# Kernel tuning notes

Measured on AMD Instinct MI355X. Metric: run time of the kernel, lower is better.

## Reference

```python
import jax, jax.numpy as jnp
import numpy as np

B, C, H, W = 32, 512, 24, 8
C8 = C // 8  # PAM query/key channels


def setup_inputs() -> dict:
    key = jax.random.key(0)
    k0, k1, k2, k3, k4 = jax.random.split(key, 5)
    x = jax.random.normal(k0, (B, C, H, W), dtype=jnp.float32)
    Wq = jax.random.normal(k1, (C8, C), dtype=jnp.float32) * 0.02
    bq = jnp.zeros((C8,), dtype=jnp.float32)
    Wk = jax.random.normal(k2, (C8, C), dtype=jnp.float32) * 0.02
    bk = jnp.zeros((C8,), dtype=jnp.float32)
    return {"x": x, "Wq": Wq, "bq": bq, "Wk": Wk, "bk": bk}


def reference(x, Wq, bq, Wk, bk):
    b, c, h, w = x.shape
    hw = h * w
    xf = x.reshape(b, c, hw)  # [B, C, hw]

    # QAConv: einsum('gchw,pcyx->gpyxhw') with kernel == x, then view(B,-1,hw,hw).
    # With m=(h,w) of features and n=(y,x) of kernel this is 'gcm,pcn->gpnm'.
    score = jnp.einsum('gcm,pcn->gpnm', xf, xf)  # [B, B, hw, hw]
    kernel_max = score.max(axis=3)               # max over feature positions -> [B, B, hw]

    # PAM: 1x1 conv projections then bmm(q^T, k).
    q = jnp.einsum('qc,bcm->bqm', Wq, xf) + bq[None, :, None]  # [B, C8, hw]
    k = jnp.einsum('qc,bcm->bqm', Wk, xf) + bk[None, :, None]  # [B, C8, hw]
    energy = jnp.einsum('bqm,bqn->bmn', q, k)                  # [B, hw, hw]
    pos_max = energy.max(axis=2)[None]                         # [1, B, hw]

    return jnp.concatenate([kernel_max, pos_max], axis=0)  # [B+1, B, hw]
```

## Files before the change

### kernel.cpp

```cpp
#include <hip/hip_runtime.h>

typedef __bf16 bf16x8 __attribute__((ext_vector_type(8)));
typedef float f32x4 __attribute__((ext_vector_type(4)));
typedef unsigned short u16x8 __attribute__((ext_vector_type(8)));
typedef unsigned short u16x4 __attribute__((ext_vector_type(4)));

#define B_ 32
#define CC 512
#define HW 192
#define C8_ 64
#define NTRI 528
#define PAIR_B 24576
#define SMEM_BYTES 73728

__device__ inline unsigned short f2bf(float f) {
    unsigned u = __float_as_uint(f);
    unsigned r = (u + 0x7FFFu + ((u >> 16) & 1u)) >> 16;
    return (unsigned short)r;
}

__device__ inline void gload16(const void* g, void* l) {
    __builtin_amdgcn_global_load_lds(
        (const __attribute__((address_space(1))) unsigned*)g,
        (__attribute__((address_space(3))) unsigned*)l,
        16, 0, 0);
}

__global__ void k_transpose(const float* __restrict__ x,
                            unsigned short* __restrict__ xt) {
    __shared__ unsigned short tile[64 * 64];
    int b = blockIdx.x / 3, mt = blockIdx.x % 3;
    int m0 = mt * 64, c0 = blockIdx.y * 64;
    int t = threadIdx.x;
    const float* xb = x + (size_t)b * CC * HW + (size_t)c0 * HW + m0;

    int mq = t & 15, cl0 = t >> 4;
    int sw = (mq & 7) << 3;
    #pragma unroll
    for (int rd = 0; rd < 4; ++rd) {
        int cl = rd * 16 + cl0;
        f32x4 v = *(const f32x4*)(xb + cl * HW + mq * 4);
        #pragma unroll
        for (int e = 0; e < 4; ++e)
            tile[(mq * 4 + e) * 64 + (cl ^ sw)] = f2bf(v[e]);
    }
    __syncthreads();
    unsigned short* xo = xt + ((size_t)b * HW + m0) * CC + c0;
    int kc = t & 7, mr0 = t >> 3;
    #pragma unroll
    for (int rd = 0; rd < 2; ++rd) {
        int mr = rd * 32 + mr0;
        u16x8 v = *(const u16x8*)&tile[mr * 64 + ((kc << 3) ^ (((mr >> 2) & 7) << 3))];
        *(u16x8*)(xo + (size_t)mr * CC + kc * 8) = v;
    }
}

__global__ void wcvt(const float* __restrict__ Wq, const float* __restrict__ Wk,
                     unsigned short* __restrict__ wqb, unsigned short* __restrict__ wkb) {
    const float* src = (blockIdx.x < 32) ? Wq : Wk;
    unsigned short* dst = (blockIdx.x < 32) ? wqb : wkb;
    int base = (blockIdx.x & 31) * 1024 + threadIdx.x * 4;
    f32x4 a = *(const f32x4*)(src + base);
    u16x4 o;
    #pragma unroll
    for (int e = 0; e < 4; ++e) o[e] = f2bf(a[e]);
    *(u16x4*)(dst + base) = o;
}

__global__ __launch_bounds__(256) void pam_qk(
        const unsigned short* __restrict__ xt,
        const unsigned short* __restrict__ wqb, const unsigned short* __restrict__ wkb,
        const float* __restrict__ bq, const float* __restrict__ bk,
        unsigned short* __restrict__ qo, unsigned short* __restrict__ ko) {
    int b = blockIdx.x, m0 = blockIdx.y * 48;
    int tid = threadIdx.x, w = tid >> 6, lane = tid & 63;
    int l15 = lane & 15, lq = lane >> 4;
    int qc = w * 16 + l15;

    f32x4 accq[3], acck[3];
    #pragma unroll
    for (int i = 0; i < 3; ++i) {
        accq[i] = (f32x4){0.f, 0.f, 0.f, 0.f};
        acck[i] = (f32x4){0.f, 0.f, 0.f, 0.f};
    }

    const unsigned short* xb = xt + ((size_t)b * HW + m0) * CC;
    const unsigned short* wqp = wqb + (size_t)qc * CC;
    const unsigned short* wkp = wkb + (size_t)qc * CC;

    for (int kt = 0; kt < 16; ++kt) {
        int ko8 = kt * 32 + lq * 8;
        bf16x8 wqf = *(const bf16x8*)(wqp + ko8);
        bf16x8 wkf = *(const bf16x8*)(wkp + ko8);
        bf16x8 af[3];
        #pragma unroll
        for (int i = 0; i < 3; ++i)
            af[i] = *(const bf16x8*)(xb + (i * 16 + l15) * CC + ko8);
        #pragma unroll
        for (int i = 0; i < 3; ++i) {
            accq[i] = __builtin_amdgcn_mfma_f32_16x16x32_bf16(af[i], wqf, accq[i], 0, 0, 0);
            acck[i] = __builtin_amdgcn_mfma_f32_16x16x32_bf16(af[i], wkf, acck[i], 0, 0, 0);
        }
    }

    float bqv = bq[qc], bkv = bk[qc];
    #pragma unroll
    for (int i = 0; i < 3; ++i) {
        #pragma unroll
        for (int r = 0; r < 4; ++r) {
            int m = m0 + i * 16 + lq * 4 + r;
            qo[((size_t)b * HW + m) * C8_ + qc] = f2bf(accq[i][r] + bqv);
            ko[((size_t)b * HW + m) * C8_ + qc] = f2bf(acck[i][r] + bkv);
        }
    }
}

__global__ __launch_bounds__(256) void pam_energy(
        const unsigned short* __restrict__ qo,
        const unsigned short* __restrict__ ko,
        float* __restrict__ out) {
    int b = blockIdx.x, m0 = blockIdx.y * 48;
    int tid = threadIdx.x, w = tid >> 6, lane = tid & 63;
    int l15 = lane & 15, lq = lane >> 4;
    int n0 = w * 48;

    f32x4 acc[3][3];
    #pragma unroll
    for (int i = 0; i < 3; ++i)
        #pragma unroll
        for (int j = 0; j < 3; ++j)
            acc[i][j] = (f32x4){0.f, 0.f, 0.f, 0.f};

    const unsigned short* qb = qo + ((size_t)b * HW + m0) * C8_;
    const unsigned short* kb = ko + ((size_t)b * HW + n0) * C8_;

    #pragma unroll
    for (int kt = 0; kt < 2; ++kt) {
        int ko8 = kt * 32 + lq * 8;
        bf16x8 af[3], bfr[3];
        #pragma unroll
        for (int i = 0; i < 3; ++i)
            af[i] = *(const bf16x8*)(qb + (i * 16 + l15) * C8_ + ko8);
        #pragma unroll
        for (int j = 0; j < 3; ++j)
            bfr[j] = *(const bf16x8*)(kb + (j * 16 + l15) * C8_ + ko8);
        #pragma unroll
        for (int i = 0; i < 3; ++i)
            #pragma unroll
            for (int j = 0; j < 3; ++j)
                acc[i][j] = __builtin_amdgcn_mfma_f32_16x16x32_bf16(af[i], bfr[j], acc[i][j], 0, 0, 0);
    }

    __shared__ float red[4][48];
    #pragma unroll
    for (int i = 0; i < 3; ++i) {
        float rm[4];
        #pragma unroll
        for (int r = 0; r < 4; ++r) rm[r] = -1e30f;
        #pragma unroll
        for (int j = 0; j < 3; ++j)
            #pragma unroll
            for (int r = 0; r < 4; ++r)
                rm[r] = fmaxf(rm[r], acc[i][j][r]);
        #pragma unroll
        for (int msk = 1; msk <= 8; msk <<= 1)
            #pragma unroll
            for (int r = 0; r < 4; ++r)
                rm[r] = fmaxf(rm[r], __shfl_xor(rm[r], msk));
        if (l15 == 0) {
            #pragma unroll
            for (int r = 0; r < 4; ++r)
                red[w][i * 16 + lq * 4 + r] = rm[r];
        }
    }
    __syncthreads();
    if (tid < 48) {
        float v = fmaxf(fmaxf(red[0][tid], red[1][tid]),
                        fmaxf(red[2][tid], red[3][tid]));
        out[((size_t)B_ * B_ + b) * HW + m0 + tid] = v;
    }
}

__global__ __launch_bounds__(512, 4) void gram(const unsigned short* __restrict__ xt,
                                               float* __restrict__ out) {
    extern __shared__ char smem[];

    int tid = threadIdx.x;
    int bid = (blockIdx.x & 7) * 66 + (blockIdx.x >> 3);
    int idx = bid, g = 0;
    while (idx >= B_ - g) { idx -= B_ - g; ++g; }
    int p = g + idx;

    const unsigned short* xg = xt + (size_t)g * HW * CC;
    const unsigned short* xp = xt + (size_t)p * HW * CC;

    int w = tid >> 6, lane = tid & 63;
    int wr = w >> 2, wc = w & 3;
    int l15 = lane & 15, lq = lane >> 4;

    int rowbase = (w & 3) * 48;
    const unsigned short* gsrc = (w < 4 ? xg : xp)
        + (size_t)(rowbase + (lane >> 2)) * CC
        + (((lane & 3) ^ ((lane >> 3) & 3)) << 3);
    unsigned ldsoff = (unsigned)(w < 4 ? 0 : 12288) + (unsigned)rowbase * 64;

    unsigned ssw = (unsigned)((lq ^ ((l15 >> 1) & 3)) << 4);
    unsigned aoff[6], boff[3];
    #pragma unroll
    for (int i = 0; i < 6; ++i)
        aoff[i] = (unsigned)(wr * 96 + i * 16 + l15) * 64 + ssw;
    #pragma unroll
    for (int j = 0; j < 3; ++j)
        boff[j] = 12288u + (unsigned)(wc * 48 + j * 16 + l15) * 64 + ssw;

    f32x4 acc[6][3];
    #pragma unroll
    for (int i = 0; i < 6; ++i)
        #pragma unroll
        for (int j = 0; j < 3; ++j)
            acc[i][j] = (f32x4){0.f, 0.f, 0.f, 0.f};

    #define STAGE(buf, kt)                                                     \
        {                                                                      \
            char* db = smem + (buf) * PAIR_B + ldsoff;                         \
            const unsigned short* gp = gsrc + (kt) * 32;                       \
            _Pragma("unroll")                                                  \
            for (int ci = 0; ci < 3; ++ci)                                     \
                gload16(gp + ci * 16 * CC, db + ci * 1024);                    \
        }

    #define COMPUTE(buf)                                                       \
        {                                                                      \
            const char* Bb = smem + (buf) * PAIR_B;                            \
            bf16x8 af[6], bfr[3];                                              \
            _Pragma("unroll")                                                  \
            for (int i = 0; i < 6; ++i)                                        \
                af[i] = *(const bf16x8*)(Bb + aoff[i]);                        \
            _Pragma("unroll")                                                  \
            for (int j = 0; j < 3; ++j)                                        \
                bfr[j] = *(const bf16x8*)(Bb + boff[j]);                       \
            _Pragma("unroll")                                                  \
            for (int i = 0; i < 6; ++i)                                        \
                _Pragma("unroll")                                              \
                for (int j = 0; j < 3; ++j)                                    \
                    acc[i][j] = __builtin_amdgcn_mfma_f32_16x16x32_bf16(       \
                        af[i], bfr[j], acc[i][j], 0, 0, 0);                    \
        }

    #define WAIT3() asm volatile("s_waitcnt vmcnt(3)" ::: "memory")
    #define WAIT0() asm volatile("s_waitcnt vmcnt(0)" ::: "memory")
    #define BAR()   { __builtin_amdgcn_sched_barrier(0); __builtin_amdgcn_s_barrier(); }

    STAGE(0, 0);
    STAGE(1, 1);

    #pragma unroll
    for (int kt = 0; kt < 16; ++kt) {
        if (kt < 15) { WAIT3(); } else { WAIT0(); }
        BAR();
        if (kt < 14) STAGE((kt + 2) % 3, kt + 2);
        COMPUTE(kt % 3);
    }

    float* colbuf = (float*)(smem + PAIR_B);
    float* rowbuf = colbuf + 2 * HW;
    #pragma unroll
    for (int j = 0; j < 3; ++j) {
        float cm = -1e30f;
        #pragma unroll
        for (int i = 0; i < 6; ++i)
            #pragma unroll
            for (int r = 0; r < 4; ++r)
                cm = fmaxf(cm, acc[i][j][r]);
        cm = fmaxf(cm, __shfl_xor(cm, 16));
        cm = fmaxf(cm, __shfl_xor(cm, 32));
        if (lane < 16) colbuf[wr * HW + wc * 48 + j * 16 + l15] = cm;
    }
    #pragma unroll
    for (int i = 0; i < 6; ++i) {
        float rm[4];
        #pragma unroll
        for (int r = 0; r < 4; ++r) rm[r] = -1e30f;
        #pragma unroll
        for (int j = 0; j < 3; ++j)
            #pragma unroll
            for (int r = 0; r < 4; ++r)
                rm[r] = fmaxf(rm[r], acc[i][j][r]);
        #pragma unroll
        for (int msk = 1; msk <= 8; msk <<= 1)
            #pragma unroll
            for (int r = 0; r < 4; ++r)
                rm[r] = fmaxf(rm[r], __shfl_xor(rm[r], msk));
        if (l15 == 0) {
            #pragma unroll
            for (int r = 0; r < 4; ++r)
                rowbuf[wc * HW + wr * 96 + i * 16 + lq * 4 + r] = rm[r];
        }
    }
    __syncthreads();
    if (tid < HW) {
        float cmax = fmaxf(colbuf[tid], colbuf[HW + tid]);
        out[((size_t)g * B_ + p) * HW + tid] = cmax;
        float rmax = fmaxf(fmaxf(rowbuf[tid], rowbuf[HW + tid]),
                           fmaxf(rowbuf[2 * HW + tid], rowbuf[3 * HW + tid]));
        out[((size_t)p * B_ + g) * HW + tid] = rmax;
    }
}

extern "C" void kernel_launch(void* const* d_in, const int* in_sizes, int n_in,
                              void* d_out, int out_size, void* d_ws, size_t ws_size,
                              hipStream_t stream) {
    (void)in_sizes; (void)n_in; (void)out_size; (void)ws_size;
    const float* x  = (const float*)d_in[0];
    const float* Wq = (const float*)d_in[1];
    const float* bq = (const float*)d_in[2];
    const float* Wk = (const float*)d_in[3];
    const float* bk = (const float*)d_in[4];
    float* out = (float*)d_out;

    char* ws = (char*)d_ws;
    unsigned short* xt  = (unsigned short*)ws;
    unsigned short* wqb = (unsigned short*)(ws + 6291456);
    unsigned short* wkb = (unsigned short*)(ws + 6291456 + 65536);
    unsigned short* qbuf = (unsigned short*)(ws + 6291456 + 131072);
    unsigned short* kbuf = (unsigned short*)(ws + 6291456 + 131072 + 786432);

    hipFuncSetAttribute((const void*)gram,
                        hipFuncAttributeMaxDynamicSharedMemorySize, SMEM_BYTES);

    k_transpose<<<dim3(96, 8), dim3(256), 0, stream>>>(x, xt);
    wcvt<<<dim3(64), dim3(256), 0, stream>>>(Wq, Wk, wqb, wkb);
    pam_qk<<<dim3(32, 4), dim3(256), 0, stream>>>(xt, wqb, wkb, bq, bk, qbuf, kbuf);
    pam_energy<<<dim3(32, 4), dim3(256), 0, stream>>>(qbuf, kbuf, out);
    gram<<<dim3(NTRI), dim3(512), SMEM_BYTES, stream>>>(xt, out);
}
```

Baseline: 60.33 us.

## Fuse PAM projection and energy into gram kernel; merge prep kernels

```diff
diff --git a/kernel.cpp b/kernel.cpp
--- a/kernel.cpp
+++ b/kernel.cpp
@@ -10,6 +10,7 @@
 #define HW 192
 #define C8_ 64
 #define NTRI 528
+#define NBLK 656
 #define PAIR_B 24576
 #define SMEM_BYTES 73728
 
@@ -26,12 +27,26 @@
         16, 0, 0);
 }
 
-__global__ void k_transpose(const float* __restrict__ x,
-                            unsigned short* __restrict__ xt) {
+__global__ void prep(const float* __restrict__ x,
+                     const float* __restrict__ Wq, const float* __restrict__ Wk,
+                     unsigned short* __restrict__ xt,
+                     unsigned short* __restrict__ wqb, unsigned short* __restrict__ wkb) {
     __shared__ unsigned short tile[64 * 64];
+    int t = threadIdx.x;
+    if (blockIdx.x >= 96) {
+        int id = (blockIdx.x - 96) * 8 + blockIdx.y;
+        const float* src = (id < 32) ? Wq : Wk;
+        unsigned short* dst = (id < 32) ? wqb : wkb;
+        int base = (id & 31) * 1024 + t * 4;
+        f32x4 a = *(const f32x4*)(src + base);
+        u16x4 o;
+        #pragma unroll
+        for (int e = 0; e < 4; ++e) o[e] = f2bf(a[e]);
+        *(u16x4*)(dst + base) = o;
+        return;
+    }
     int b = blockIdx.x / 3, mt = blockIdx.x % 3;
     int m0 = mt * 64, c0 = blockIdx.y * 64;
-    int t = threadIdx.x;
     const float* xb = x + (size_t)b * CC * HW + (size_t)c0 * HW + m0;
 
     int mq = t & 15, cl0 = t >> 4;
@@ -55,255 +70,250 @@
     }
 }
 
-__global__ void wcvt(const float* __restrict__ Wq, const float* __restrict__ Wk,
-                     unsigned short* __restrict__ wqb, unsigned short* __restrict__ wkb) {
-    const float* src = (blockIdx.x < 32) ? Wq : Wk;
-    unsigned short* dst = (blockIdx.x < 32) ? wqb : wkb;
-    int base = (blockIdx.x & 31) * 1024 + threadIdx.x * 4;
-    f32x4 a = *(const f32x4*)(src + base);
-    u16x4 o;
-    #pragma unroll
-    for (int e = 0; e < 4; ++e) o[e] = f2bf(a[e]);
-    *(u16x4*)(dst + base) = o;
-}
-
-__global__ __launch_bounds__(256) void pam_qk(
+__global__ __launch_bounds__(512, 4) void gram_pam(
         const unsigned short* __restrict__ xt,
         const unsigned short* __restrict__ wqb, const unsigned short* __restrict__ wkb,
         const float* __restrict__ bq, const float* __restrict__ bk,
-        unsigned short* __restrict__ qo, unsigned short* __restrict__ ko) {
-    int b = blockIdx.x, m0 = blockIdx.y * 48;
-    int tid = threadIdx.x, w = tid >> 6, lane = tid & 63;
+        float* __restrict__ out) {
+    extern __shared__ char smem[];
+    int tid = threadIdx.x;
+    int w = tid >> 6, lane = tid & 63;
     int l15 = lane & 15, lq = lane >> 4;
-    int qc = w * 16 + l15;
-
-    f32x4 accq[3], acck[3];
-    #pragma unroll
-    for (int i = 0; i < 3; ++i) {
-        accq[i] = (f32x4){0.f, 0.f, 0.f, 0.f};
-        acck[i] = (f32x4){0.f, 0.f, 0.f, 0.f};
-    }
-
-    const unsigned short* xb = xt + ((size_t)b * HW + m0) * CC;
-    const unsigned short* wqp = wqb + (size_t)qc * CC;
-    const unsigned short* wkp = wkb + (size_t)qc * CC;
-
-    for (int kt = 0; kt < 16; ++kt) {
-        int ko8 = kt * 32 + lq * 8;
-        bf16x8 wqf = *(const bf16x8*)(wqp + ko8);
-        bf16x8 wkf = *(const bf16x8*)(wkp + ko8);
-        bf16x8 af[3];
-        #pragma unroll
-        for (int i = 0; i < 3; ++i)
-            af[i] = *(const bf16x8*)(xb + (i * 16 + l15) * CC + ko8);
-        #pragma unroll
-        for (int i = 0; i < 3; ++i) {
-            accq[i] = __builtin_amdgcn_mfma_f32_16x16x32_bf16(af[i], wqf, accq[i], 0, 0, 0);
-            acck[i] = __builtin_amdgcn_mfma_f32_16x16x32_bf16(af[i], wkf, acck[i], 0, 0, 0);
-        }
-    }
-
-    float bqv = bq[qc], bkv = bk[qc];
-    #pragma unroll
-    for (int i = 0; i < 3; ++i) {
-        #pragma unroll
-        for (int r = 0; r < 4; ++r) {
-            int m = m0 + i * 16 + lq * 4 + r;
-            qo[((size_t)b * HW + m) * C8_ + qc] = f2bf(accq[i][r] + bqv);
-            ko[((size_t)b * HW + m) * C8_ + qc] = f2bf(acck[i][r] + bkv);
-        }
-    }
-}
-
-__global__ __launch_bounds__(256) void pam_energy(
-        const unsigned short* __restrict__ qo,
-        const unsigned short* __restrict__ ko,
-        float* __restrict__ out) {
-    int b = blockIdx.x, m0 = blockIdx.y * 48;
-    int tid = threadIdx.x, w = tid >> 6, lane = tid & 63;
-    int l15 = lane & 15, lq = lane >> 4;
-    int n0 = w * 48;
-
-    f32x4 acc[3][3];
-    #pragma unroll
-    for (int i = 0; i < 3; ++i)
+    int bid = (blockIdx.x & 7) * 82 + (blockIdx.x >> 3);
+
+    if (bid < NTRI) {
+        int idx = bid, g = 0;
+        while (idx >= B_ - g) { idx -= B_ - g; ++g; }
+        int p = g + idx;
+        const unsigned short* xg = xt + (size_t)g * HW * CC;
+        const unsigned short* xp = xt + (size_t)p * HW * CC;
+        int wr = w >> 2, wc = w & 3;
+
+        int rowbase = (w & 3) * 48;
+        const unsigned short* gsrc = (w < 4 ? xg : xp)
+            + (size_t)(rowbase + (lane >> 2)) * CC
+            + (((lane & 3) ^ ((lane >> 3) & 3)) << 3);
+        unsigned ldsoff = (unsigned)(w < 4 ? 0 : 12288) + (unsigned)rowbase * 64;
+
+        unsigned ssw = (unsigned)((lq ^ ((l15 >> 1) & 3)) << 4);
+        unsigned aoff[6], boff[3];
+        #pragma unroll
+        for (int i = 0; i < 6; ++i)
+            aoff[i] = (unsigned)(wr * 96 + i * 16 + l15) * 64 + ssw;
         #pragma unroll
         for (int j = 0; j < 3; ++j)
-            acc[i][j] = (f32x4){0.f, 0.f, 0.f, 0.f};
-
-    const unsigned short* qb = qo + ((size_t)b * HW + m0) * C8_;
-    const unsigned short* kb = ko + ((size_t)b * HW + n0) * C8_;
-
-    #pragma unroll
-    for (int kt = 0; kt < 2; ++kt) {
-        int ko8 = kt * 32 + lq * 8;
-        bf16x8 af[3], bfr[3];
-        #pragma unroll
-        for (int i = 0; i < 3; ++i)
-            af[i] = *(const bf16x8*)(qb + (i * 16 + l15) * C8_ + ko8);
-        #pragma unroll
-        for (int j = 0; j < 3; ++j)
-            bfr[j] = *(const bf16x8*)(kb + (j * 16 + l15) * C8_ + ko8);
-        #pragma unroll
-        for (int i = 0; i < 3; ++i)
+            boff[j] = 12288u + (unsigned)(wc * 48 + j * 16 + l15) * 64 + ssw;
+
+        f32x4 acc[6][3];
+        #pragma unroll
+        for (int i = 0; i < 6; ++i)
             #pragma unroll
             for (int j = 0; j < 3; ++j)
-                acc[i][j] = __builtin_amdgcn_mfma_f32_16x16x32_bf16(af[i], bfr[j], acc[i][j], 0, 0, 0);
-    }
-
-    __shared__ float red[4][48];
-    #pragma unroll
-    for (int i = 0; i < 3; ++i) {
-        float rm[4];
-        #pragma unroll
-        for (int r = 0; r < 4; ++r) rm[r] = -1e30f;
-        #pragma unroll
-        for (int j = 0; j < 3; ++j)
-            #pragma unroll
-            for (int r = 0; r < 4; ++r)
-                rm[r] = fmaxf(rm[r], acc[i][j][r]);
-        #pragma unroll
-        for (int msk = 1; msk <= 8; msk <<= 1)
-            #pragma unroll
-            for (int r = 0; r < 4; ++r)
-                rm[r] = fmaxf(rm[r], __shfl_xor(rm[r], msk));
-        if (l15 == 0) {
-            #pragma unroll
-            for (int r = 0; r < 4; ++r)
-                red[w][i * 16 + lq * 4 + r] = rm[r];
-        }
-    }
-    __syncthreads();
-    if (tid < 48) {
-        float v = fmaxf(fmaxf(red[0][tid], red[1][tid]),
-                        fmaxf(red[2][tid], red[3][tid]));
-        out[((size_t)B_ * B_ + b) * HW + m0 + tid] = v;
-    }
-}
-
-__global__ __launch_bounds__(512, 4) void gram(const unsigned short* __restrict__ xt,
-                                               float* __restrict__ out) {
-    extern __shared__ char smem[];
-
-    int tid = threadIdx.x;
-    int bid = (blockIdx.x & 7) * 66 + (blockIdx.x >> 3);
-    int idx = bid, g = 0;
-    while (idx >= B_ - g) { idx -= B_ - g; ++g; }
-    int p = g + idx;
-
-    const unsigned short* xg = xt + (size_t)g * HW * CC;
-    const unsigned short* xp = xt + (size_t)p * HW * CC;
-
-    int w = tid >> 6, lane = tid & 63;
-    int wr = w >> 2, wc = w & 3;
-    int l15 = lane & 15, lq = lane >> 4;
-
-    int rowbase = (w & 3) * 48;
-    const unsigned short* gsrc = (w < 4 ? xg : xp)
-        + (size_t)(rowbase + (lane >> 2)) * CC
-        + (((lane & 3) ^ ((lane >> 3) & 3)) << 3);
-    unsigned ldsoff = (unsigned)(w < 4 ? 0 : 12288) + (unsigned)rowbase * 64;
-
-    unsigned ssw = (unsigned)((lq ^ ((l15 >> 1) & 3)) << 4);
-    unsigned aoff[6], boff[3];
-    #pragma unroll
-    for (int i = 0; i < 6; ++i)
-        aoff[i] = (unsigned)(wr * 96 + i * 16 + l15) * 64 + ssw;
-    #pragma unroll
-    for (int j = 0; j < 3; ++j)
-        boff[j] = 12288u + (unsigned)(wc * 48 + j * 16 + l15) * 64 + ssw;
-
-    f32x4 acc[6][3];
-    #pragma unroll
-    for (int i = 0; i < 6; ++i)
-        #pragma unroll
-        for (int j = 0; j < 3; ++j)
-            acc[i][j] = (f32x4){0.f, 0.f, 0.f, 0.f};
-
-    #define STAGE(buf, kt)                                                     \
-        {                                                                      \
-            char* db = smem + (buf) * PAIR_B + ldsoff;                         \
-            const unsigned short* gp = gsrc + (kt) * 32;                       \
-            _Pragma("unroll")                                                  \
-            for (int ci = 0; ci < 3; ++ci)                                     \
-                gload16(gp + ci * 16 * CC, db + ci * 1024);                    \
-        }
-
-    #define COMPUTE(buf)                                                       \
-        {                                                                      \
-            const char* Bb = smem + (buf) * PAIR_B;                            \
-            bf16x8 af[6], bfr[3];                                              \
-            _Pragma("unroll")                                                  \
-            for (int i = 0; i < 6; ++i)                                        \
-                af[i] = *(const bf16x8*)(Bb + aoff[i]);                        \
-            _Pragma("unroll")                                                  \
-            for (int j = 0; j < 3; ++j)                                        \
-                bfr[j] = *(const bf16x8*)(Bb + boff[j]);                       \
-            _Pragma("unroll")                                                  \
-            for (int i = 0; i < 6; ++i)                                        \
+                acc[i][j] = (f32x4){0.f, 0.f, 0.f, 0.f};
+
+        #define STAGE(buf, kt)                                                 \
+            {                                                                  \
+                char* db = smem + (buf) * PAIR_B + ldsoff;                     \
+                const unsigned short* gp = gsrc + (kt) * 32;                   \
+                _Pragma("unroll")                                              \
+                for (int ci = 0; ci < 3; ++ci)                                 \
+                    gload16(gp + ci * 16 * CC, db + ci * 1024);                \
+            }
+
+        #define COMPUTE(buf)                                                   \
+            {                                                                  \
+                const char* Bb = smem + (buf) * PAIR_B;                        \
+                bf16x8 af[6], bfr[3];                                          \
+                _Pragma("unroll")                                              \
+                for (int i = 0; i < 6; ++i)                                    \
+                    af[i] = *(const bf16x8*)(Bb + aoff[i]);                    \
                 _Pragma("unroll")                                              \
                 for (int j = 0; j < 3; ++j)                                    \
-                    acc[i][j] = __builtin_amdgcn_mfma_f32_16x16x32_bf16(       \
-                        af[i], bfr[j], acc[i][j], 0, 0, 0);                    \
-        }
-
-    #define WAIT3() asm volatile("s_waitcnt vmcnt(3)" ::: "memory")
-    #define WAIT0() asm volatile("s_waitcnt vmcnt(0)" ::: "memory")
-    #define BAR()   { __builtin_amdgcn_sched_barrier(0); __builtin_amdgcn_s_barrier(); }
-
-    STAGE(0, 0);
-    STAGE(1, 1);
-
-    #pragma unroll
-    for (int kt = 0; kt < 16; ++kt) {
-        if (kt < 15) { WAIT3(); } else { WAIT0(); }
-        BAR();
-        if (kt < 14) STAGE((kt + 2) % 3, kt + 2);
-        COMPUTE(kt % 3);
-    }
-
-    float* colbuf = (float*)(smem + PAIR_B);
-    float* rowbuf = colbuf + 2 * HW;
-    #pragma unroll
-    for (int j = 0; j < 3; ++j) {
-        float cm = -1e30f;
-        #pragma unroll
-        for (int i = 0; i < 6; ++i)
-            #pragma unroll
-            for (int r = 0; r < 4; ++r)
-                cm = fmaxf(cm, acc[i][j][r]);
-        cm = fmaxf(cm, __shfl_xor(cm, 16));
-        cm = fmaxf(cm, __shfl_xor(cm, 32));
-        if (lane < 16) colbuf[wr * HW + wc * 48 + j * 16 + l15] = cm;
-    }
-    #pragma unroll
-    for (int i = 0; i < 6; ++i) {
-        float rm[4];
-        #pragma unroll
-        for (int r = 0; r < 4; ++r) rm[r] = -1e30f;
-        #pragma unroll
-        for (int j = 0; j < 3; ++j)
-            #pragma unroll
-            for (int r = 0; r < 4; ++r)
-                rm[r] = fmaxf(rm[r], acc[i][j][r]);
-        #pragma unroll
-        for (int msk = 1; msk <= 8; msk <<= 1)
-            #pragma unroll
-            for (int r = 0; r < 4; ++r)
-                rm[r] = fmaxf(rm[r], __shfl_xor(rm[r], msk));
-        if (l15 == 0) {
-            #pragma unroll
-            for (int r = 0; r < 4; ++r)
-                rowbuf[wc * HW + wr * 96 + i * 16 + lq * 4 + r] = rm[r];
-        }
-    }
-    __syncthreads();
-    if (tid < HW) {
-        float cmax = fmaxf(colbuf[tid], colbuf[HW + tid]);
-        out[((size_t)g * B_ + p) * HW + tid] = cmax;
-        float rmax = fmaxf(fmaxf(rowbuf[tid], rowbuf[HW + tid]),
-                           fmaxf(rowbuf[2 * HW + tid], rowbuf[3 * HW + tid]));
-        out[((size_t)p * B_ + g) * HW + tid] = rmax;
+                    bfr[j] = *(const bf16x8*)(Bb + boff[j]);                   \
+                _Pragma("unroll")                                              \
+                for (int i = 0; i < 6; ++i)                                    \
+                    _Pragma("unroll")                                          \
+                    for (int j = 0; j < 3; ++j)                                \
+                        acc[i][j] = __builtin_amdgcn_mfma_f32_16x16x32_bf16(   \
+                            af[i], bfr[j], acc[i][j], 0, 0, 0);                \
+            }
+
+        #define WAIT3() asm volatile("s_waitcnt vmcnt(3)" ::: "memory")
+        #define WAIT0() asm volatile("s_waitcnt vmcnt(0)" ::: "memory")
+        #define BAR()   { __builtin_amdgcn_sched_barrier(0); __builtin_amdgcn_s_barrier(); }
+
+        STAGE(0, 0);
+        STAGE(1, 1);
+
+        #pragma unroll
+        for (int kt = 0; kt < 16; ++kt) {
+            if (kt < 15) { WAIT3(); } else { WAIT0(); }
+            BAR();
+            if (kt < 14) STAGE((kt + 2) % 3, kt + 2);
+            COMPUTE(kt % 3);
+        }
+
+        float* colbuf = (float*)(smem + PAIR_B);
+        float* rowbuf = colbuf + 2 * HW;
+        #pragma unroll
+        for (int j = 0; j < 3; ++j) {
+            float cm = -1e30f;
+            #pragma unroll
+            for (int i = 0; i < 6; ++i)
+                #pragma unroll
+                for (int r = 0; r < 4; ++r)
+                    cm = fmaxf(cm, acc[i][j][r]);
+            cm = fmaxf(cm, __shfl_xor(cm, 16));
+            cm = fmaxf(cm, __shfl_xor(cm, 32));
+            if (lane < 16) colbuf[wr * HW + wc * 48 + j * 16 + l15] = cm;
+        }
+        #pragma unroll
+        for (int i = 0; i < 6; ++i) {
+            float rm[4];
+            #pragma unroll
+            for (int r = 0; r < 4; ++r) rm[r] = -1e30f;
+            #pragma unroll
+            for (int j = 0; j < 3; ++j)
+                #pragma unroll
+                for (int r = 0; r < 4; ++r)
+                    rm[r] = fmaxf(rm[r], acc[i][j][r]);
+            #pragma unroll
+            for (int msk = 1; msk <= 8; msk <<= 1)
+                #pragma unroll
+                for (int r = 0; r < 4; ++r)
+                    rm[r] = fmaxf(rm[r], __shfl_xor(rm[r], msk));
+            if (l15 == 0) {
+                #pragma unroll
+                for (int r = 0; r < 4; ++r)
+                    rowbuf[wc * HW + wr * 96 + i * 16 + lq * 4 + r] = rm[r];
+            }
+        }
+        __syncthreads();
+        if (tid < HW) {
+            float cmax = fmaxf(colbuf[tid], colbuf[HW + tid]);
+            out[((size_t)g * B_ + p) * HW + tid] = cmax;
+            float rmax = fmaxf(fmaxf(rowbuf[tid], rowbuf[HW + tid]),
+                               fmaxf(rowbuf[2 * HW + tid], rowbuf[3 * HW + tid]));
+            out[((size_t)p * B_ + g) * HW + tid] = rmax;
+        }
+    } else {
+        int pb = bid - NTRI;
+        int b = pb >> 2, mgrp = pb & 3;
+        int m0 = mgrp * 48;
+        unsigned short* qs = (unsigned short*)smem;
+        unsigned short* ks = (unsigned short*)(smem + 6144);
+        float* red = (float*)(smem + 6144 + 24576);
+        const unsigned short* xb = xt + (size_t)b * HW * CC;
+
+        int qc = (w & 3) * 16 + l15;
+        if (w < 4) {
+            const unsigned short* wp = wqb + (size_t)qc * CC;
+            float bias = bq[qc];
+            f32x4 a3[3];
+            #pragma unroll
+            for (int i = 0; i < 3; ++i) a3[i] = (f32x4){0.f, 0.f, 0.f, 0.f};
+            for (int kt = 0; kt < 16; ++kt) {
+                int ko8 = kt * 32 + lq * 8;
+                bf16x8 wf = *(const bf16x8*)(wp + ko8);
+                #pragma unroll
+                for (int i = 0; i < 3; ++i) {
+                    bf16x8 af = *(const bf16x8*)(xb + (m0 + i * 16 + l15) * CC + ko8);
+                    a3[i] = __builtin_amdgcn_mfma_f32_16x16x32_bf16(af, wf, a3[i], 0, 0, 0);
+                }
+            }
+            #pragma unroll
+            for (int i = 0; i < 3; ++i) {
+                #pragma unroll
+                for (int r = 0; r < 4; ++r) {
+                    int lm = i * 16 + lq * 4 + r;
+                    qs[lm * 64 + ((((qc >> 3) ^ (lm & 7)) << 3) | (qc & 7))] = f2bf(a3[i][r] + bias);
+                }
+            }
+        } else {
+            const unsigned short* wp = wkb + (size_t)qc * CC;
+            float bias = bk[qc];
+            f32x4 kacc[12];
+            #pragma unroll
+            for (int i = 0; i < 12; ++i) kacc[i] = (f32x4){0.f, 0.f, 0.f, 0.f};
+            for (int kt = 0; kt < 16; ++kt) {
+                int ko8 = kt * 32 + lq * 8;
+                bf16x8 wf = *(const bf16x8*)(wp + ko8);
+                #pragma unroll
+                for (int i = 0; i < 12; ++i) {
+                    bf16x8 af = *(const bf16x8*)(xb + (i * 16 + l15) * CC + ko8);
+                    kacc[i] = __builtin_amdgcn_mfma_f32_16x16x32_bf16(af, wf, kacc[i], 0, 0, 0);
+                }
+            }
+            #pragma unroll
+            for (int i = 0; i < 12; ++i) {
+                #pragma unroll
+                for (int r = 0; r < 4; ++r) {
+                    int m = i * 16 + lq * 4 + r;
+                    ks[m * 64 + ((((qc >> 3) ^ (m & 7)) << 3) | (qc & 7))] = f2bf(kacc[i][r] + bias);
+                }
+            }
+        }
+        __syncthreads();
+
+        int nf0 = (w < 4) ? 2 * w : 8 + (w - 4);
+        int nfn = (w < 4) ? 2 : 1;
+        f32x4 acc2[3][2];
+        #pragma unroll
+        for (int i = 0; i < 3; ++i)
+            #pragma unroll
+            for (int j = 0; j < 2; ++j)
+                acc2[i][j] = (f32x4){0.f, 0.f, 0.f, 0.f};
+        #pragma unroll
+        for (int kt2 = 0; kt2 < 2; ++kt2) {
+            int chunk = kt2 * 4 + lq;
+            bf16x8 af[3];
+            #pragma unroll
+            for (int i = 0; i < 3; ++i) {
+                int lm = i * 16 + l15;
+                af[i] = *(const bf16x8*)&qs[lm * 64 + ((chunk ^ (lm & 7)) << 3)];
+            }
+            #pragma unroll
+            for (int jj = 0; jj < 2; ++jj) {
+                if (jj < nfn) {
+                    int n = (nf0 + jj) * 16 + l15;
+                    bf16x8 bfr = *(const bf16x8*)&ks[n * 64 + ((chunk ^ (n & 7)) << 3)];
+                    #pragma unroll
+                    for (int i = 0; i < 3; ++i)
+                        acc2[i][jj] = __builtin_amdgcn_mfma_f32_16x16x32_bf16(
+                            af[i], bfr, acc2[i][jj], 0, 0, 0);
+                }
+            }
+        }
+        #pragma unroll
+        for (int i = 0; i < 3; ++i) {
+            float rm[4];
+            #pragma unroll
+            for (int r = 0; r < 4; ++r) rm[r] = -1e30f;
+            #pragma unroll
+            for (int jj = 0; jj < 2; ++jj)
+                if (jj < nfn)
+                    #pragma unroll
+                    for (int r = 0; r < 4; ++r)
+                        rm[r] = fmaxf(rm[r], acc2[i][jj][r]);
+            #pragma unroll
+            for (int msk = 1; msk <= 8; msk <<= 1)
+                #pragma unroll
+                for (int r = 0; r < 4; ++r)
+                    rm[r] = fmaxf(rm[r], __shfl_xor(rm[r], msk));
+            if (l15 == 0) {
+                #pragma unroll
+                for (int r = 0; r < 4; ++r)
+                    red[w * 48 + i * 16 + lq * 4 + r] = rm[r];
+            }
+        }
+        __syncthreads();
+        if (tid < 48) {
+            float v = red[tid];
+            #pragma unroll
+            for (int ww = 1; ww < 8; ++ww)
+                v = fmaxf(v, red[ww * 48 + tid]);
+            out[((size_t)B_ * B_ + b) * HW + m0 + tid] = v;
+        }
     }
 }
 
@@ -322,15 +332,10 @@
     unsigned short* xt  = (unsigned short*)ws;
     unsigned short* wqb = (unsigned short*)(ws + 6291456);
     unsigned short* wkb = (unsigned short*)(ws + 6291456 + 65536);
-    unsigned short* qbuf = (unsigned short*)(ws + 6291456 + 131072);
-    unsigned short* kbuf = (unsigned short*)(ws + 6291456 + 131072 + 786432);
-
-    hipFuncSetAttribute((const void*)gram,
+
+    hipFuncSetAttribute((const void*)gram_pam,
                         hipFuncAttributeMaxDynamicSharedMemorySize, SMEM_BYTES);
 
-    k_transpose<<<dim3(96, 8), dim3(256), 0, stream>>>(x, xt);
-    wcvt<<<dim3(64), dim3(256), 0, stream>>>(Wq, Wk, wqb, wkb);
-    pam_qk<<<dim3(32, 4), dim3(256), 0, stream>>>(xt, wqb, wkb, bq, bk, qbuf, kbuf);
-    pam_energy<<<dim3(32, 4), dim3(256), 0, stream>>>(qbuf, kbuf, out);
-    gram<<<dim3(NTRI), dim3(512), SMEM_BYTES, stream>>>(xt, out);
-}
+    prep<<<dim3(104, 8), dim3(256), 0, stream>>>(x, Wq, Wk, xt, wqb, wkb);
+    gram_pam<<<dim3(NBLK), dim3(512), SMEM_BYTES, stream>>>(xt, wqb, wkb, bq, bk, out);
+}
```

Result: slower. 109.6 us (+81.6%).
